# Performance work log

Hardware: AMD Instinct MI355X
Metric: run time of the kernel (lower is better)

The kernel has to match this reference:

```python
import jax, jax.numpy as jnp
import numpy as np

EPS = 1e-5


def hetero_layernorm(x, node_type, gamma, beta):
    # LayerNorm over feature dim with per-node-type affine params.
    mu = jnp.mean(x, axis=-1, keepdims=True)
    var = jnp.mean(jnp.square(x - mu), axis=-1, keepdims=True)
    xn = (x - mu) * jax.lax.rsqrt(var + EPS)
    return xn * gamma[node_type] + beta[node_type]


def rgcn_conv(y, edge_src, edge_dst, edge_type, W_rel, W_root):
    # Transform per relation first (R small), then gather per-edge message.
    n = y.shape[0]
    h = jnp.einsum('nd,rde->rne', y, W_rel)          # [R, N, d]
    msg = h[edge_type, edge_src]                     # [E, d] gather
    agg = jax.ops.segment_sum(msg, edge_dst, num_segments=n)  # [N, d]
    return agg + y @ W_root


def hetero_mlp(y, node_type, W_mlp, b_mlp):
    # Per-node-type linear: compute for all T types, then select.
    n = y.shape[0]
    h = jnp.einsum('nd,tde->tne', y, W_mlp) + b_mlp[:, None, :]  # [T, N, d]
    return h[node_type, jnp.arange(n)]


def setup_inputs() -> dict:
    key = jax.random.key(0)
    ks = jax.random.split(key, 8)
    N, E, D, T, R = 50000, 800000, 128, 4, 8
    x = jax.random.normal(ks[0], (N, D), dtype=jnp.float32)
    edge_src = jax.random.randint(ks[1], (E,), 0, N, dtype=jnp.int32)
    edge_dst = jax.random.randint(ks[2], (E,), 0, N, dtype=jnp.int32)
    node_type = jax.random.randint(ks[3], (N,), 0, T, dtype=jnp.int32)
    edge_type = jax.random.randint(ks[4], (E,), 0, R, dtype=jnp.int32)
    # Scale weights ~ 1/sqrt(fan_in) for stable magnitudes.
    s = 1.0 / np.sqrt(D)
    W_rel = jax.random.normal(ks[5], (R, D, D), dtype=jnp.float32) * s
    W_root = jax.random.normal(ks[6], (D, D), dtype=jnp.float32) * s
    W_mlp = jax.random.normal(ks[7], (T, D, D), dtype=jnp.float32) * s
    return {
        'x': x, 'edge_src': edge_src, 'edge_dst': edge_dst,
        'node_type': node_type, 'edge_type': edge_type,
        'conv_gamma': jnp.ones((T, D), jnp.float32),
        'conv_beta': jnp.zeros((T, D), jnp.float32),
        'W_rel': W_rel, 'W_root': W_root,
        'mlp_gamma': jnp.ones((T, D), jnp.float32),
        'mlp_beta': jnp.zeros((T, D), jnp.float32),
        'W_mlp': W_mlp, 'b_mlp': jnp.zeros((T, D), jnp.float32),
    }


def reference(x, edge_src, edge_dst, node_type, edge_type,
              conv_gamma, conv_beta, W_rel, W_root,
              mlp_gamma, mlp_beta, W_mlp, b_mlp):
    # Norm -> Act -> (Dropout p=0, eval) -> Conv -> Residual
    y = hetero_layernorm(x, node_type, conv_gamma, conv_beta)
    y = jax.nn.relu(y)
    x = x + rgcn_conv(y, edge_src, edge_dst, edge_type, W_rel, W_root)
    # Norm -> Act -> (Dropout p=0, eval) -> MLP -> Residual
    y = hetero_layernorm(x, node_type, mlp_gamma, mlp_beta)
    y = jax.nn.relu(y)
    x = x + hetero_mlp(y, node_type, W_mlp, b_mlp)
    return x
```

## Files before the change

kernel.cpp:

```cpp
#include <hip/hip_runtime.h>
#include <hip/hip_bf16.h>

#define D 128
#define EPS 1e-5f
#define CHK 8192
#define P2CAP 6144

typedef __attribute__((ext_vector_type(8))) short short8;
typedef __attribute__((ext_vector_type(4))) float float4v;

#define AS1 __attribute__((address_space(1)))
#define AS3 __attribute__((address_space(3)))

__device__ inline ushort f2bf(float f) {
    __hip_bfloat16 b = __float2bfloat16(f);
    return *reinterpret_cast<ushort*>(&b);
}
__device__ inline float bf_lo(uint u) { return __uint_as_float(u << 16); }
__device__ inline float bf_hi(uint u) { return __uint_as_float(u & 0xffff0000u); }

__global__ void k_ln1cvt(const float* __restrict__ x, const int* __restrict__ ntp,
                         const float* __restrict__ gamma, const float* __restrict__ beta,
                         ushort* __restrict__ y,
                         const float* __restrict__ Wrel, const float* __restrict__ Wroot,
                         const float* __restrict__ Wmlp, ushort* __restrict__ Wt, int N) {
    __shared__ ushort t[128][136];
    if (blockIdx.x < 13) {
        int m = blockIdx.x;
        const float* src = (m == 0) ? Wroot
                         : (m <= 8) ? Wrel + (size_t)(m - 1) * D * D
                                    : Wmlp + (size_t)(m - 9) * D * D;
        for (int i = threadIdx.x; i < D * D; i += 256) {
            int k = i >> 7, n = i & 127;
            t[n][k] = f2bf(src[i]);
        }
        __syncthreads();
        ushort* dst = Wt + (size_t)m * D * D;
        for (int i = threadIdx.x; i < D * D; i += 256) {
            int frag = i >> 9;
            int lane = (i >> 3) & 63;
            int j = i & 7;
            int nt = frag >> 2, ks = frag & 3;
            int n = nt * 16 + (lane & 15);
            int k = ks * 32 + (lane >> 4) * 8 + j;
            dst[i] = t[n][k];
        }
        return;
    }
    int n = (blockIdx.x - 13) * 4 + (threadIdx.x >> 6);
    if (n >= N) return;
    int l = threadIdx.x & 63;
    float2 v = *(const float2*)(x + (size_t)n * D + 2 * l);
    float s = v.x + v.y, s2 = v.x * v.x + v.y * v.y;
    #pragma unroll
    for (int o = 32; o; o >>= 1) { s += __shfl_xor(s, o, 64); s2 += __shfl_xor(s2, o, 64); }
    float mu = s * (1.0f / D);
    float var = s2 * (1.0f / D) - mu * mu;
    float inv = rsqrtf(var + EPS);
    int tt = ntp[n];
    float2 g = *(const float2*)(gamma + tt * D + 2 * l);
    float2 b = *(const float2*)(beta + tt * D + 2 * l);
    float a0 = fmaxf((v.x - mu) * inv * g.x + b.x, 0.0f);
    float a1 = fmaxf((v.y - mu) * inv * g.y + b.y, 0.0f);
    ((uint*)(y + (size_t)n * D))[l] = ((uint)f2bf(a1) << 16) | f2bf(a0);
}

__global__ void k_c1(const int* __restrict__ edst, int* __restrict__ hist, int E, int B) {
    __shared__ int cnt[256];
    int c = blockIdx.x, tid = threadIdx.x;
    cnt[tid] = 0;
    __syncthreads();
    #pragma unroll 4
    for (int k = 0; k < CHK / 256; ++k) {
        int e = c * CHK + k * 256 + tid;
        if (e < E) atomicAdd(&cnt[edst[e] >> 8], 1);
    }
    __syncthreads();
    if (tid < B) hist[c * B + tid] = cnt[tid];
}
__global__ void k_c2(const int* __restrict__ hist, int* __restrict__ chunkoff,
                     int* __restrict__ bucktot, int C, int B) {
    __shared__ int v[128];
    int b = blockIdx.x, t = threadIdx.x;
    v[t] = (t < C) ? hist[t * B + b] : 0;
    __syncthreads();
    if (t == 0) {
        int s = 0;
        for (int c = 0; c < C; ++c) { int x = v[c]; v[c] = s; s += x; }
        bucktot[b] = s;
    }
    __syncthreads();
    if (t < C) chunkoff[t * B + b] = v[t];
}
__global__ void k_p1s(const int* __restrict__ edst, const int* __restrict__ esrc,
                      const int* __restrict__ etyp, const int* __restrict__ bucktot,
                      const int* __restrict__ chunkoff, uint* __restrict__ edata,
                      int E, int B) {
    __shared__ int ps[256];
    __shared__ int base[256];
    __shared__ int cnt[256];
    int c = blockIdx.x, tid = threadIdx.x;
    int bt = (tid < B) ? bucktot[tid] : 0;
    ps[tid] = bt;
    __syncthreads();
    for (int o = 1; o < 256; o <<= 1) {
        int v = (tid >= o) ? ps[tid - o] : 0;
        __syncthreads();
        ps[tid] += v;
        __syncthreads();
    }
    base[tid] = (ps[tid] - bt) + ((tid < B) ? chunkoff[c * B + tid] : 0);
    cnt[tid] = 0;
    __syncthreads();
    #pragma unroll 4
    for (int k = 0; k < CHK / 256; ++k) {
        int e = c * CHK + k * 256 + tid;
        if (e < E) {
            int d = edst[e];
            int b = d >> 8;
            int r = atomicAdd(&cnt[b], 1);
            edata[base[b] + r] =
                ((uint)esrc[e] << 12) | ((uint)(d & 255) << 4) | (uint)etyp[e];
        }
    }
}
__global__ void k_p2(const uint* __restrict__ edata, const int* __restrict__ bucktot,
                     uint* __restrict__ epack, int* __restrict__ offs,
                     int N, int E, int B) {
    __shared__ int ps[256];
    __shared__ uint ed[P2CAP];
    __shared__ int cnt[256], off[256], cur[256];
    int b = blockIdx.x, tid = threadIdx.x;
    int bt = (tid < B) ? bucktot[tid] : 0;
    ps[tid] = bt;
    __syncthreads();
    for (int o = 1; o < 256; o <<= 1) {
        int v = (tid >= o) ? ps[tid - o] : 0;
        __syncthreads();
        ps[tid] += v;
        __syncthreads();
    }
    int j0 = ps[b] - ((b < B) ? bucktot[b] : 0);
    int count = ps[b] - j0;
    if (count > P2CAP) count = P2CAP;
    for (int i = tid; i < count; i += 256) ed[i] = edata[j0 + i];
    cnt[tid] = 0;
    __syncthreads();
    for (int i = tid; i < count; i += 256) atomicAdd(&cnt[(ed[i] >> 4) & 255], 1);
    __syncthreads();
    if (tid == 0) {
        int s = 0;
        for (int i = 0; i < 256; ++i) { off[i] = s; cur[i] = s; s += cnt[i]; }
    }
    __syncthreads();
    for (int i = tid; i < count; i += 256) {
        uint v = ed[i];
        int dl = (v >> 4) & 255;
        int r = atomicAdd(&cur[dl], 1);
        epack[j0 + r] = ((v & 15u) << 28) | (v >> 12);
    }
    int v = b * 256 + tid;
    if (v < N) offs[v] = j0 + off[tid];
    if (b == 0 && tid == 0) offs[N] = E;
}

__global__ void k_zagg(const ushort* __restrict__ ybuf, const int* __restrict__ offs,
                       const uint* __restrict__ epack, ushort* __restrict__ zbuf, int N) {
    int wave = threadIdx.x >> 6;
    int l = threadIdx.x & 63;
    int v = blockIdx.x * 4 + wave;
    if (v >= N) return;
    float2 a0 = {0.f,0.f}, a1 = {0.f,0.f}, a2 = {0.f,0.f}, a3 = {0.f,0.f};
    float2 a4 = {0.f,0.f}, a5 = {0.f,0.f}, a6 = {0.f,0.f}, a7 = {0.f,0.f};
    const uint* yb = (const uint*)ybuf;
    int j = offs[v], e1 = offs[v + 1];

#define ZACC(P, U) do {                                                   \
        float lo = bf_lo(U), hi = bf_hi(U);                               \
        switch ((P) >> 28) {                                              \
            case 0: a0.x += lo; a0.y += hi; break;                        \
            case 1: a1.x += lo; a1.y += hi; break;                        \
            case 2: a2.x += lo; a2.y += hi; break;                        \
            case 3: a3.x += lo; a3.y += hi; break;                        \
            case 4: a4.x += lo; a4.y += hi; break;                        \
            case 5: a5.x += lo; a5.y += hi; break;                        \
            case 6: a6.x += lo; a6.y += hi; break;                        \
            default: a7.x += lo; a7.y += hi; break;                       \
        }                                                                 \
    } while (0)

    while (j < e1) {
        int chunk = min(64, e1 - j);
        uint pl = (j + l < e1) ? epack[j + l] : 0;
        for (int i = 0; i < chunk; i += 16) {
            uint pp[16], uu[16];
            #pragma unroll
            for (int k = 0; k < 16; ++k)
                pp[k] = (i + k < chunk) ? __shfl(pl, i + k, 64) : 0u;
            #pragma unroll
            for (int k = 0; k < 16; ++k)
                uu[k] = (i + k < chunk) ? yb[(size_t)(pp[k] & 0x0FFFFFFFu) * 64 + l] : 0u;
            #pragma unroll
            for (int k = 0; k < 16; ++k) ZACC(pp[k], uu[k]);
        }
        j += chunk;
    }
#undef ZACC
    uint* zrow = (uint*)(zbuf + (size_t)v * 1024);
    zrow[0 * 64 + l] = ((uint)f2bf(a0.y) << 16) | f2bf(a0.x);
    zrow[1 * 64 + l] = ((uint)f2bf(a1.y) << 16) | f2bf(a1.x);
    zrow[2 * 64 + l] = ((uint)f2bf(a2.y) << 16) | f2bf(a2.x);
    zrow[3 * 64 + l] = ((uint)f2bf(a3.y) << 16) | f2bf(a3.x);
    zrow[4 * 64 + l] = ((uint)f2bf(a4.y) << 16) | f2bf(a4.x);
    zrow[5 * 64 + l] = ((uint)f2bf(a5.y) << 16) | f2bf(a5.x);
    zrow[6 * 64 + l] = ((uint)f2bf(a6.y) << 16) | f2bf(a6.x);
    zrow[7 * 64 + l] = ((uint)f2bf(a7.y) << 16) | f2bf(a7.x);
}

__device__ __forceinline__ void gl_lds16(const void* g, void* l) {
    __builtin_amdgcn_global_load_lds((const AS1 void*)g, (AS3 void*)l, 16, 0, 0);
}
__device__ __forceinline__ void stage_half(const ushort* __restrict__ Wt, int q,
                                           ushort* bsm0, int wave, int lane) {
    const char* g = (const char*)Wt + (size_t)q * 16384 + lane * 16;
    char* l = (char*)bsm0 + (q & 1) * 16384;
    #pragma unroll
    for (int i = 0; i < 4; ++i) {
        int c = i * 4 + wave;
        gl_lds16(g + c * 1024, l + c * 1024);
    }
}
__device__ __forceinline__ void stage_mlp_slice(const ushort* __restrict__ Wt, int nt,
                                                ushort* bsm0, int wave, int lane) {
    const char* g = (const char*)Wt + (size_t)(9 + wave) * 32768 + nt * 4096 + lane * 16;
    char* l = (char*)bsm0 + (nt & 1) * 16384 + wave * 4096;
    #pragma unroll
    for (int i = 0; i < 4; ++i)
        gl_lds16(g + i * 1024, l + i * 1024);
}
__device__ __forceinline__ void aloadG(short8 (&d)[4], const ushort* p, int off, int ao) {
    #pragma unroll
    for (int ks = 0; ks < 4; ++ks)
        d[ks] = *(const short8*)(p + off + ks * 32 + ao);
}
__device__ __forceinline__ void convHalf(float4v (&acc)[8], const short8 (&a)[4],
                                         const ushort* bsm_h, int h, int lane) {
    #pragma unroll
    for (int nt4 = 0; nt4 < 4; ++nt4) {
        #pragma unroll
        for (int ks = 0; ks < 4; ++ks) {
            short8 b = *(const short8*)(bsm_h + (((nt4 * 4 + ks) * 64 + lane) << 3));
            acc[h * 4 + nt4] = __builtin_amdgcn_mfma_f32_16x16x32_bf16(
                a[ks], b, acc[h * 4 + nt4], 0, 0, 0);
        }
    }
}

__launch_bounds__(256, 4)
__global__ void k_gm(const ushort* __restrict__ ybuf, const ushort* __restrict__ zbuf,
                     const ushort* __restrict__ Wt, const float* __restrict__ x,
                     const int* __restrict__ ntp,
                     const float* __restrict__ gamma, const float* __restrict__ beta,
                     const float* __restrict__ bmlp, float* __restrict__ out, int N) {
    __shared__ ushort bsm[2][8192];
    ushort* bsm0 = &bsm[0][0];
    int tid = threadIdx.x;
    int wave = tid >> 6, lane = tid & 63;
    int quad = lane >> 4, l15 = lane & 15;
    int ao = quad * 8;
    int base = blockIdx.x * 64 + wave * 16;

    const ushort* yrow = ybuf + (size_t)min(base + l15, N - 1) * 128;
    const ushort* zrow = zbuf + (size_t)min(base + l15, N - 1) * 1024;

    float4v acc[8];
    #pragma unroll
    for (int nt = 0; nt < 8; ++nt) acc[nt] = (float4v){0.f, 0.f, 0.f, 0.f};

    short8 aC[4], aN[4];
    stage_half(Wt, 0, bsm0, wave, lane);
    aloadG(aC, yrow, 0, ao);
    __syncthreads();

    #pragma unroll
    for (int m = 0; m < 9; ++m) {
        short8 (&cur)[4] = (m & 1) ? aN : aC;
        short8 (&nxt)[4] = (m & 1) ? aC : aN;
        stage_half(Wt, 2 * m + 1, bsm0, wave, lane);
        if (m < 8) aloadG(nxt, zrow, m * 128, ao);
        convHalf(acc, cur, bsm0, 0, lane);
        __syncthreads();
        if (m < 8) stage_half(Wt, 2 * m + 2, bsm0, wave, lane);
        else       stage_mlp_slice(Wt, 0, bsm0, wave, lane);
        convHalf(acc, cur, bsm0 + 8192, 1, lane);
        __syncthreads();
    }

    ushort* yov = bsm0 + 8192 + wave * 2048;
    int ty[4];
    {
        float s[4] = {0.f, 0.f, 0.f, 0.f}, s2[4] = {0.f, 0.f, 0.f, 0.f};
        #pragma unroll
        for (int nt = 0; nt < 8; ++nt) {
            int col = nt * 16 + l15;
            #pragma unroll
            for (int r = 0; r < 4; ++r) {
                int row = base + quad * 4 + r;
                float xv = (row < N) ? x[(size_t)row * D + col] : 0.f;
                float t = acc[nt][r] + xv;
                acc[nt][r] = t;
                s[r] += t; s2[r] += t * t;
            }
        }
        #pragma unroll
        for (int r = 0; r < 4; ++r) {
            #pragma unroll
            for (int o = 1; o < 16; o <<= 1) {
                s[r]  += __shfl_xor(s[r],  o, 64);
                s2[r] += __shfl_xor(s2[r], o, 64);
            }
        }
        #pragma unroll
        for (int r = 0; r < 4; ++r) {
            int rc = min(base + quad * 4 + r, N - 1);
            ty[r] = ntp[rc];
            float mu  = s[r] * (1.0f / D);
            float var = s2[r] * (1.0f / D) - mu * mu;
            float inv = rsqrtf(var + EPS);
            int lrow = quad * 4 + r;
            #pragma unroll
            for (int nt = 0; nt < 8; ++nt) {
                int col = nt * 16 + l15;
                float yn = fmaxf((acc[nt][r] - mu) * inv * gamma[ty[r] * D + col]
                                 + beta[ty[r] * D + col], 0.f);
                yov[lrow * 128 + col] = f2bf(yn);
            }
        }
    }
    short8 a2[4];
    {
        const ushort* myrow = yov + l15 * 128;
        #pragma unroll
        for (int ks = 0; ks < 4; ++ks) a2[ks] = *(const short8*)(myrow + ks * 32 + ao);
    }
    __syncthreads();

    #pragma unroll
    for (int nt = 0; nt < 8; ++nt) {
        if (nt < 7) stage_mlp_slice(Wt, nt + 1, bsm0, wave, lane);
        const ushort* bh = bsm0 + (nt & 1) * 8192;
        float4v c0 = {0.f,0.f,0.f,0.f}, c1 = {0.f,0.f,0.f,0.f};
        float4v c2 = {0.f,0.f,0.f,0.f}, c3 = {0.f,0.f,0.f,0.f};
        #pragma unroll
        for (int ks = 0; ks < 4; ++ks) {
            int fo = (ks * 64 + lane) << 3;
            short8 b0 = *(const short8*)(bh + 0 * 2048 + fo);
            short8 b1 = *(const short8*)(bh + 1 * 2048 + fo);
            short8 b2 = *(const short8*)(bh + 2 * 2048 + fo);
            short8 b3 = *(const short8*)(bh + 3 * 2048 + fo);
            c0 = __builtin_amdgcn_mfma_f32_16x16x32_bf16(a2[ks], b0, c0, 0, 0, 0);
            c1 = __builtin_amdgcn_mfma_f32_16x16x32_bf16(a2[ks], b1, c1, 0, 0, 0);
            c2 = __builtin_amdgcn_mfma_f32_16x16x32_bf16(a2[ks], b2, c2, 0, 0, 0);
            c3 = __builtin_amdgcn_mfma_f32_16x16x32_bf16(a2[ks], b3, c3, 0, 0, 0);
        }
        int col = nt * 16 + l15;
        #pragma unroll
        for (int r = 0; r < 4; ++r) {
            int row = base + quad * 4 + r;
            if (row < N) {
                int t = ty[r];
                float v = (t == 0) ? c0[r] : (t == 1) ? c1[r] : (t == 2) ? c2[r] : c3[r];
                out[(size_t)row * D + col] = acc[nt][r] + v + bmlp[t * D + col];
            }
        }
        if (nt < 7) __syncthreads();
    }
}

extern "C" void kernel_launch(void* const* d_in, const int* in_sizes, int n_in,
                              void* d_out, int out_size, void* d_ws, size_t ws_size,
                              hipStream_t stream) {
    const float* x          = (const float*)d_in[0];
    const int*   esrc       = (const int*)d_in[1];
    const int*   edst       = (const int*)d_in[2];
    const int*   ntyp       = (const int*)d_in[3];
    const int*   etyp       = (const int*)d_in[4];
    const float* conv_gamma = (const float*)d_in[5];
    const float* conv_beta  = (const float*)d_in[6];
    const float* W_rel      = (const float*)d_in[7];
    const float* W_root     = (const float*)d_in[8];
    const float* mlp_gamma  = (const float*)d_in[9];
    const float* mlp_beta   = (const float*)d_in[10];
    const float* W_mlp      = (const float*)d_in[11];
    const float* b_mlp      = (const float*)d_in[12];
    float* out = (float*)d_out;

    int N = in_sizes[0] / D;
    int E = in_sizes[1];
    int C = (E + CHK - 1) / CHK;
    int B = (N + 255) / 256;

    char* p = (char*)d_ws;
    auto take = [&p](size_t bytes) { char* q = p; p += (bytes + 255) & ~(size_t)255; return q; };
    ushort* ybuf    = (ushort*)take((size_t)N * D * 2);
    ushort* zbuf    = (ushort*)take((size_t)N * 1024 * 2);
    ushort* Wt      = (ushort*)take((size_t)13 * D * D * 2);
    uint*   edata   = (uint*)take((size_t)E * 4);
    uint*   epack   = (uint*)take((size_t)E * 4);
    int*    offs    = (int*)take((size_t)(N + 1) * 4);
    int*    hist    = (int*)take((size_t)C * B * 4);
    int*    chunkoff= (int*)take((size_t)C * B * 4);
    int*    bucktot = (int*)take((size_t)B * 4);

    k_ln1cvt<<<13 + (N + 3) / 4, 256, 0, stream>>>(x, ntyp, conv_gamma, conv_beta,
                                                   ybuf, W_rel, W_root, W_mlp, Wt, N);

    k_c1<<<C, 256, 0, stream>>>(edst, hist, E, B);
    k_c2<<<B, 128, 0, stream>>>(hist, chunkoff, bucktot, C, B);
    k_p1s<<<C, 256, 0, stream>>>(edst, esrc, etyp, bucktot, chunkoff, edata, E, B);
    k_p2<<<B, 256, 0, stream>>>(edata, bucktot, epack, offs, N, E, B);

    k_zagg<<<(N + 3) / 4, 256, 0, stream>>>(ybuf, offs, epack, zbuf, N);

    k_gm<<<(N + 63) / 64, 256, 0, stream>>>(ybuf, zbuf, Wt, x, ntyp,
                                            mlp_gamma, mlp_beta, b_mlp, out, N);
}
```

Measured before the change: 279.1 us.

## Fuse per-relation neighbor aggregation into GEMM kernel, sort edges by (dst, relation)

The k_p2 edge sort now orders edges by destination and relation and writes per-(node, relation) offsets, so each relation segment is contiguous. The separate k_zagg kernel and its large bf16 zbuf intermediate are removed. The GEMM kernel instead gathers and sums neighbor rows per relation into shared memory, interleaved with the MFMA loop, which avoids writing and re-reading about 100MB of intermediate data. In exchange, the gather runs with serial per-node loops inside the GEMM waves, uses extra LDS, and lowers the occupancy hint from 4 to 3.

```diff
diff --git a/kernel.cpp b/kernel.cpp
--- a/kernel.cpp
+++ b/kernel.cpp
@@ -125,11 +125,11 @@
     }
 }
 __global__ void k_p2(const uint* __restrict__ edata, const int* __restrict__ bucktot,
-                     uint* __restrict__ epack, int* __restrict__ offs,
+                     uint* __restrict__ epack, int* __restrict__ offs2,
                      int N, int E, int B) {
     __shared__ int ps[256];
     __shared__ uint ed[P2CAP];
-    __shared__ int cnt[256], off[256], cur[256];
+    __shared__ int cnt[2048], off[2048], cur[2048];
     int b = blockIdx.x, tid = threadIdx.x;
     int bt = (tid < B) ? bucktot[tid] : 0;
     ps[tid] = bt;
@@ -144,77 +144,47 @@
     int count = ps[b] - j0;
     if (count > P2CAP) count = P2CAP;
     for (int i = tid; i < count; i += 256) ed[i] = edata[j0 + i];
-    cnt[tid] = 0;
-    __syncthreads();
-    for (int i = tid; i < count; i += 256) atomicAdd(&cnt[(ed[i] >> 4) & 255], 1);
-    __syncthreads();
-    if (tid == 0) {
-        int s = 0;
-        for (int i = 0; i < 256; ++i) { off[i] = s; cur[i] = s; s += cnt[i]; }
-    }
+    #pragma unroll
+    for (int j = 0; j < 8; ++j) cnt[tid * 8 + j] = 0;
     __syncthreads();
     for (int i = tid; i < count; i += 256) {
         uint v = ed[i];
-        int dl = (v >> 4) & 255;
-        int r = atomicAdd(&cur[dl], 1);
-        epack[j0 + r] = ((v & 15u) << 28) | (v >> 12);
-    }
-    int v = b * 256 + tid;
-    if (v < N) offs[v] = j0 + off[tid];
-    if (b == 0 && tid == 0) offs[N] = E;
-}
-
-__global__ void k_zagg(const ushort* __restrict__ ybuf, const int* __restrict__ offs,
-                       const uint* __restrict__ epack, ushort* __restrict__ zbuf, int N) {
-    int wave = threadIdx.x >> 6;
-    int l = threadIdx.x & 63;
-    int v = blockIdx.x * 4 + wave;
-    if (v >= N) return;
-    float2 a0 = {0.f,0.f}, a1 = {0.f,0.f}, a2 = {0.f,0.f}, a3 = {0.f,0.f};
-    float2 a4 = {0.f,0.f}, a5 = {0.f,0.f}, a6 = {0.f,0.f}, a7 = {0.f,0.f};
-    const uint* yb = (const uint*)ybuf;
-    int j = offs[v], e1 = offs[v + 1];
-
-#define ZACC(P, U) do {                                                   \
-        float lo = bf_lo(U), hi = bf_hi(U);                               \
-        switch ((P) >> 28) {                                              \
-            case 0: a0.x += lo; a0.y += hi; break;                        \
-            case 1: a1.x += lo; a1.y += hi; break;                        \
-            case 2: a2.x += lo; a2.y += hi; break;                        \
-            case 3: a3.x += lo; a3.y += hi; break;                        \
-            case 4: a4.x += lo; a4.y += hi; break;                        \
-            case 5: a5.x += lo; a5.y += hi; break;                        \
-            case 6: a6.x += lo; a6.y += hi; break;                        \
-            default: a7.x += lo; a7.y += hi; break;                       \
-        }                                                                 \
-    } while (0)
-
-    while (j < e1) {
-        int chunk = min(64, e1 - j);
-        uint pl = (j + l < e1) ? epack[j + l] : 0;
-        for (int i = 0; i < chunk; i += 16) {
-            uint pp[16], uu[16];
-            #pragma unroll
-            for (int k = 0; k < 16; ++k)
-                pp[k] = (i + k < chunk) ? __shfl(pl, i + k, 64) : 0u;
-            #pragma unroll
-            for (int k = 0; k < 16; ++k)
-                uu[k] = (i + k < chunk) ? yb[(size_t)(pp[k] & 0x0FFFFFFFu) * 64 + l] : 0u;
-            #pragma unroll
-            for (int k = 0; k < 16; ++k) ZACC(pp[k], uu[k]);
-        }
-        j += chunk;
-    }
-#undef ZACC
-    uint* zrow = (uint*)(zbuf + (size_t)v * 1024);
-    zrow[0 * 64 + l] = ((uint)f2bf(a0.y) << 16) | f2bf(a0.x);
-    zrow[1 * 64 + l] = ((uint)f2bf(a1.y) << 16) | f2bf(a1.x);
-    zrow[2 * 64 + l] = ((uint)f2bf(a2.y) << 16) | f2bf(a2.x);
-    zrow[3 * 64 + l] = ((uint)f2bf(a3.y) << 16) | f2bf(a3.x);
-    zrow[4 * 64 + l] = ((uint)f2bf(a4.y) << 16) | f2bf(a4.x);
-    zrow[5 * 64 + l] = ((uint)f2bf(a5.y) << 16) | f2bf(a5.x);
-    zrow[6 * 64 + l] = ((uint)f2bf(a6.y) << 16) | f2bf(a6.x);
-    zrow[7 * 64 + l] = ((uint)f2bf(a7.y) << 16) | f2bf(a7.x);
+        int kk = (((v >> 4) & 255) << 3) | (v & 7);
+        atomicAdd(&cnt[kk], 1);
+    }
+    __syncthreads();
+    int loc[8], tot = 0;
+    #pragma unroll
+    for (int j = 0; j < 8; ++j) { loc[j] = tot; tot += cnt[tid * 8 + j]; }
+    __syncthreads();
+    ps[tid] = tot;
+    __syncthreads();
+    for (int o = 1; o < 256; o <<= 1) {
+        int v = (tid >= o) ? ps[tid - o] : 0;
+        __syncthreads();
+        ps[tid] += v;
+        __syncthreads();
+    }
+    int ex = ps[tid] - tot;
+    #pragma unroll
+    for (int j = 0; j < 8; ++j) {
+        off[tid * 8 + j] = ex + loc[j];
+        cur[tid * 8 + j] = ex + loc[j];
+    }
+    __syncthreads();
+    for (int i = tid; i < count; i += 256) {
+        uint v = ed[i];
+        int kk = (((v >> 4) & 255) << 3) | (v & 7);
+        int r = atomicAdd(&cur[kk], 1);
+        epack[j0 + r] = v >> 12;
+    }
+    #pragma unroll
+    for (int j = 0; j < 8; ++j) {
+        int kk = tid * 8 + j;
+        int v = b * 256 + (kk >> 3);
+        if (v < N) offs2[(size_t)b * 2048 + kk] = j0 + off[kk];
+    }
+    if (b == 0 && tid == 0) offs2[(size_t)N * 8] = E;
 }
 
 __device__ __forceinline__ void gl_lds16(const void* g, void* l) {
@@ -255,23 +225,49 @@
         }
     }
 }
-
-__launch_bounds__(256, 4)
-__global__ void k_gm(const ushort* __restrict__ ybuf, const ushort* __restrict__ zbuf,
+__device__ __forceinline__ void gatherZ(short8 (&d)[4], const uint* __restrict__ yb,
+                                        const uint* __restrict__ epack,
+                                        const int* __restrict__ offs2,
+                                        uint* ztw, int vbase, int r,
+                                        int lane, int l15, int ao, int N) {
+    for (int i = 0; i < 16; ++i) {
+        int v = vbase + i;
+        float lo = 0.f, hi = 0.f;
+        if (v < N) {
+            int o0 = offs2[(v << 3) + r];
+            int o1 = offs2[(v << 3) + r + 1];
+            uint u = (o0 < o1) ? yb[(size_t)epack[o0] * 64 + lane] : 0u;
+            for (int e = o0; e < o1; ++e) {
+                uint un = (e + 1 < o1) ? yb[(size_t)epack[e + 1] * 64 + lane] : 0u;
+                lo += bf_lo(u); hi += bf_hi(u);
+                u = un;
+            }
+        }
+        ztw[i * 68 + lane] = ((uint)f2bf(hi) << 16) | f2bf(lo);
+    }
+    const ushort* zr = (const ushort*)ztw + l15 * 136;
+    #pragma unroll
+    for (int ks = 0; ks < 4; ++ks) d[ks] = *(const short8*)(zr + ks * 32 + ao);
+}
+
+__launch_bounds__(256, 3)
+__global__ void k_gm(const ushort* __restrict__ ybuf, const uint* __restrict__ epack,
+                     const int* __restrict__ offs2,
                      const ushort* __restrict__ Wt, const float* __restrict__ x,
                      const int* __restrict__ ntp,
                      const float* __restrict__ gamma, const float* __restrict__ beta,
                      const float* __restrict__ bmlp, float* __restrict__ out, int N) {
     __shared__ ushort bsm[2][8192];
+    __shared__ uint zt[4][16 * 68];
     ushort* bsm0 = &bsm[0][0];
     int tid = threadIdx.x;
     int wave = tid >> 6, lane = tid & 63;
     int quad = lane >> 4, l15 = lane & 15;
     int ao = quad * 8;
     int base = blockIdx.x * 64 + wave * 16;
+    const uint* yb = (const uint*)ybuf;
 
     const ushort* yrow = ybuf + (size_t)min(base + l15, N - 1) * 128;
-    const ushort* zrow = zbuf + (size_t)min(base + l15, N - 1) * 1024;
 
     float4v acc[8];
     #pragma unroll
@@ -287,12 +283,13 @@
         short8 (&cur)[4] = (m & 1) ? aN : aC;
         short8 (&nxt)[4] = (m & 1) ? aC : aN;
         stage_half(Wt, 2 * m + 1, bsm0, wave, lane);
-        if (m < 8) aloadG(nxt, zrow, m * 128, ao);
         convHalf(acc, cur, bsm0, 0, lane);
         __syncthreads();
         if (m < 8) stage_half(Wt, 2 * m + 2, bsm0, wave, lane);
         else       stage_mlp_slice(Wt, 0, bsm0, wave, lane);
         convHalf(acc, cur, bsm0 + 8192, 1, lane);
+        if (m < 8) gatherZ(nxt, yb, epack, offs2, &zt[wave][0],
+                           base, m, lane, l15, ao, N);
         __syncthreads();
     }
 
@@ -403,11 +400,10 @@
     char* p = (char*)d_ws;
     auto take = [&p](size_t bytes) { char* q = p; p += (bytes + 255) & ~(size_t)255; return q; };
     ushort* ybuf    = (ushort*)take((size_t)N * D * 2);
-    ushort* zbuf    = (ushort*)take((size_t)N * 1024 * 2);
     ushort* Wt      = (ushort*)take((size_t)13 * D * D * 2);
     uint*   edata   = (uint*)take((size_t)E * 4);
     uint*   epack   = (uint*)take((size_t)E * 4);
-    int*    offs    = (int*)take((size_t)(N + 1) * 4);
+    int*    offs2   = (int*)take(((size_t)N * 8 + 1) * 4);
     int*    hist    = (int*)take((size_t)C * B * 4);
     int*    chunkoff= (int*)take((size_t)C * B * 4);
     int*    bucktot = (int*)take((size_t)B * 4);
@@ -418,10 +414,8 @@
     k_c1<<<C, 256, 0, stream>>>(edst, hist, E, B);
     k_c2<<<B, 128, 0, stream>>>(hist, chunkoff, bucktot, C, B);
     k_p1s<<<C, 256, 0, stream>>>(edst, esrc, etyp, bucktot, chunkoff, edata, E, B);
-    k_p2<<<B, 256, 0, stream>>>(edata, bucktot, epack, offs, N, E, B);
-
-    k_zagg<<<(N + 3) / 4, 256, 0, stream>>>(ybuf, offs, epack, zbuf, N);
-
-    k_gm<<<(N + 63) / 64, 256, 0, stream>>>(ybuf, zbuf, Wt, x, ntyp,
+    k_p2<<<B, 256, 0, stream>>>(edata, bucktot, epack, offs2, N, E, B);
+
+    k_gm<<<(N + 63) / 64, 256, 0, stream>>>(ybuf, epack, offs2, Wt, x, ntyp,
                                             mlp_gamma, mlp_beta, b_mlp, out, N);
 }
```

Result: slower. 535.8 us (+91.9%).
